# Kernel tuning notes

Measured on AMD Instinct MI355X. Metric: run time of the kernel, lower is better.

## Reference

```python
import jax, jax.numpy as jnp
import numpy as np

DIM = 256
HEADS = 8
WS = 7                      # window size
N = WS * WS                 # tokens per window = 49
SCALE = (DIM // HEADS) ** -0.5
B_ = 4096                   # total windows (64 images * 64 windows)
NW = 64                     # windows per image (mask.shape[0])


def _rel_index():
    # Swin relative position index, computed exactly as in the torch module.
    coords = np.stack(np.meshgrid(np.arange(WS), np.arange(WS), indexing='ij'))  # [2,WS,WS]
    cf = coords.reshape(2, -1)                          # [2, N]
    rel = cf[:, :, None] - cf[:, None, :]               # [2, N, N]
    rel = rel.transpose(1, 2, 0).copy()                 # [N, N, 2]
    rel[:, :, 0] += WS - 1
    rel[:, :, 1] += WS - 1
    rel[:, :, 0] *= 2 * WS - 1
    return rel.sum(-1)                                  # [N, N] in [0, (2WS-1)^2)


def setup_inputs() -> dict:
    key = jax.random.key(0)
    ks = jax.random.split(key, 7)
    x = jax.random.normal(ks[0], (B_, N, DIM), dtype=jnp.float32)
    mask = jax.random.normal(ks[1], (NW, N, N), dtype=jnp.float32)
    qkv_w = jax.random.normal(ks[2], (3 * DIM, DIM), dtype=jnp.float32) * 0.02
    qkv_b = jax.random.normal(ks[3], (3 * DIM,), dtype=jnp.float32) * 0.02
    proj_w = jax.random.normal(ks[4], (DIM, DIM), dtype=jnp.float32) * 0.02
    proj_b = jax.random.normal(ks[5], (DIM,), dtype=jnp.float32) * 0.02
    bias_table = jax.random.normal(ks[6], ((2 * WS - 1) ** 2, HEADS), dtype=jnp.float32) * 0.02
    rel_idx = jnp.asarray(_rel_index(), dtype=jnp.int32)
    return {"x": x, "mask": mask, "qkv_w": qkv_w, "qkv_b": qkv_b,
            "proj_w": proj_w, "proj_b": proj_b, "bias_table": bias_table,
            "rel_idx": rel_idx}


def reference(x, mask, qkv_w, qkv_b, proj_w, proj_b, bias_table, rel_idx):
    Bw, n, C = x.shape
    hd = C // HEADS
    # fused qkv projection: [Bw, n, 3C] -> [3, Bw, H, n, hd]
    qkv = (x @ qkv_w.T + qkv_b).reshape(Bw, n, 3, HEADS, hd).transpose(2, 0, 3, 1, 4)
    q, k, v = qkv[0] * SCALE, qkv[1], qkv[2]
    attn = jnp.einsum('bhnd,bhmd->bhnm', q, k)                     # [Bw,H,n,n]
    # relative position bias gather: [n*n, H] -> [H, n, n]
    bias = bias_table[rel_idx.reshape(-1)].reshape(n, n, HEADS).transpose(2, 0, 1)
    attn = attn + bias[None]
    nW = mask.shape[0]
    # shift mask add: group windows per image
    attn = attn.reshape(Bw // nW, nW, HEADS, n, n) + mask[None, :, None]
    attn = jax.nn.softmax(attn.reshape(Bw, HEADS, n, n), axis=-1)
    out = jnp.einsum('bhnm,bhmd->bhnd', attn, v)                   # [Bw,H,n,hd]
    out = out.transpose(0, 2, 1, 3).reshape(Bw, n, C)
    return out @ proj_w.T + proj_b
```

## Files before the change

kernel.cpp:

```cpp
#include <hip/hip_runtime.h>
#include <hip/hip_bf16.h>

#define NTOK 49
#define DIM 256
#define HEADS 8
#define HD 32
#define SCALE 0.17677669529663687f

typedef float f32x4 __attribute__((ext_vector_type(4)));
typedef short bf16x8 __attribute__((ext_vector_type(8)));

__device__ __forceinline__ unsigned short f2bf(float f) {
    union { __hip_bfloat16 h; unsigned short u; } c;
    c.h = __float2bfloat16(f);
    return c.u;
}
__device__ __forceinline__ float bf2f(unsigned short u) {
    return __builtin_bit_cast(float, (unsigned)u << 16);
}
__device__ __forceinline__ uint2 pack4(float a, float b, float c, float d) {
    uint2 r;
    r.x = (unsigned)f2bf(a) | ((unsigned)f2bf(b) << 16);
    r.y = (unsigned)f2bf(c) | ((unsigned)f2bf(d) << 16);
    return r;
}

__global__ void k0_prep(const float* __restrict__ qkv_w, const float* __restrict__ proj_w,
                        const float* __restrict__ mask, const float* __restrict__ bias_table,
                        const int* __restrict__ rel_idx,
                        unsigned short* __restrict__ wqf, unsigned short* __restrict__ wpf,
                        unsigned short* __restrict__ bmf, int total)
{
    int i = blockIdx.x * 256 + threadIdx.x;
    if (i >= total) return;
    if (i < 196608) {
        int j = i & 7, q = i >> 3;
        int lane = q & 63; q >>= 6;
        int ks2 = q & 7;  q >>= 3;
        int tt = q % 6;   q /= 6;
        int h  = q;
        int n96 = tt * 16 + (lane & 15);
        int seg = n96 >> 5, ch = n96 & 31;
        wqf[i] = f2bf(qkv_w[(seg * 256 + h * HD + ch) * 256 + ks2 * 32 + (lane >> 4) * 8 + j]);
    } else if (i < 262144) {
        int u = i - 196608;
        int j = u & 7, q = u >> 3;
        int lane = q & 63; q >>= 6;
        int ks2 = q & 7;  q >>= 3;
        int bt = q;
        int n = (bt >> 3) * 128 + (bt & 7) * 16 + (lane & 15);
        wpf[u] = f2bf(proj_w[n * 256 + ks2 * 32 + (lane >> 4) * 8 + j]);
    } else {
        int u = i - 262144;
        int j = u & 3;
        int lane = (u >> 2) & 63;
        int g = u >> 8;
        int mt = g & 3, ct = (g >> 2) & 3, h = (g >> 4) & 7, ws = g >> 7;
        int q = ct * 16 + (lane & 15);
        int key = mt * 16 + ((lane >> 4) & 3) * 4 + j;
        float v = 0.f;
        if (q < NTOK && key < NTOK)
            v = mask[ws * 2401 + q * NTOK + key] + bias_table[rel_idx[q * NTOK + key] * HEADS + h];
        bmf[u] = f2bf(v);
    }
}

__global__ __launch_bounds__(256, 2)
void k1_fused(
    const float* __restrict__ x,
    const float* __restrict__ qkv_b,
    const float* __restrict__ pb,
    const unsigned short* __restrict__ wqf,
    const unsigned short* __restrict__ wpf,
    const unsigned short* __restrict__ bmf,
    float* __restrict__ out)
{
    __shared__ unsigned short pool[37440];
    unsigned short* const xs = pool;

    const int t = threadIdx.x, bw = blockIdx.x;
    const int lane = t & 63, wv = t >> 6;
    const int l15 = lane & 15, l16 = lane >> 4;
    unsigned short* const qw  = pool + 12544 + wv * 6224;
    unsigned short* const kw  = qw + 1960;
    unsigned short* const vtw = qw + 3920;
    unsigned short* const pw2 = qw;

    const float* xw = x + (size_t)bw * NTOK * DIM;
    for (int cidx = t; cidx < NTOK * 32; cidx += 256) {
        int row = cidx >> 5, c8 = cidx & 31;
        float4 a = *(const float4*)(xw + row * DIM + c8 * 8);
        float4 b = *(const float4*)(xw + row * DIM + c8 * 8 + 4);
        bf16x8 v;
        v[0] = (short)f2bf(a.x); v[1] = (short)f2bf(a.y);
        v[2] = (short)f2bf(a.z); v[3] = (short)f2bf(a.w);
        v[4] = (short)f2bf(b.x); v[5] = (short)f2bf(b.y);
        v[6] = (short)f2bf(b.z); v[7] = (short)f2bf(b.w);
        *(bf16x8*)(xs + row * 256 + ((c8 * 8) ^ ((row & 7) << 3))) = v;
    }
    __syncthreads();

    int arow[4];
    #pragma unroll
    for (int i4 = 0; i4 < 4; ++i4) {
        int r = i4 * 16 + l15;
        arow[i4] = r > 48 ? 48 : r;
    }

    uint2 ob[2][2][4];

    #pragma unroll
    for (int hh = 0; hh < 2; ++hh) {
        const int h = wv + 4 * hh;
        const unsigned short* wb = wqf + (size_t)h * 24576;
        uint2 bmu[4][4];

        #pragma unroll
        for (int p = 0; p < 2; ++p) {
            f32x4 aq[4], ak[4], av[4];
            #pragma unroll
            for (int nt = 0; nt < 4; ++nt) {
                aq[nt] = (f32x4){0.f,0.f,0.f,0.f};
                ak[nt] = (f32x4){0.f,0.f,0.f,0.f};
                av[nt] = (f32x4){0.f,0.f,0.f,0.f};
            }
            __builtin_amdgcn_s_setprio(1);
            #pragma unroll
            for (int ks2 = 0; ks2 < 8; ++ks2) {
                bf16x8 xf[4];
                #pragma unroll
                for (int nt = 0; nt < 4; ++nt)
                    xf[nt] = *(const bf16x8*)(xs + arow[nt] * 256 +
                               ((ks2 * 32 + l16 * 8) ^ ((arow[nt] & 7) << 3)));
                bf16x8 wqf_ = *(const bf16x8*)(wb + ((p    ) * 8 + ks2) * 512 + lane * 8);
                bf16x8 wkf_ = *(const bf16x8*)(wb + ((2 + p) * 8 + ks2) * 512 + lane * 8);
                bf16x8 wvf_ = *(const bf16x8*)(wb + ((4 + p) * 8 + ks2) * 512 + lane * 8);
                #pragma unroll
                for (int nt = 0; nt < 4; ++nt) {
                    aq[nt] = __builtin_amdgcn_mfma_f32_16x16x32_bf16(wqf_, xf[nt], aq[nt], 0, 0, 0);
                    ak[nt] = __builtin_amdgcn_mfma_f32_16x16x32_bf16(wkf_, xf[nt], ak[nt], 0, 0, 0);
                    av[nt] = __builtin_amdgcn_mfma_f32_16x16x32_bf16(xf[nt], wvf_, av[nt], 0, 0, 0);
                }
            }
            __builtin_amdgcn_s_setprio(0);

            if (p == 0) {
                #pragma unroll
                for (int ct = 0; ct < 4; ++ct)
                    #pragma unroll
                    for (int mt = 0; mt < 4; ++mt)
                        bmu[ct][mt] = *(const uint2*)(bmf +
                            (((size_t)(((bw & 63) * 8 + h) * 16 + ct * 4 + mt)) << 8) + (lane << 2));
            }

            float4 bq4 = *(const float4*)(qkv_b + h * HD + p * 16 + l16 * 4);
            float4 bk4 = *(const float4*)(qkv_b + 256 + h * HD + p * 16 + l16 * 4);
            float  bvs = qkv_b[512 + h * HD + p * 16 + l15];
            #pragma unroll
            for (int nt = 0; nt < 4; ++nt) {
                int tok = nt * 16 + l15;
                if (tok < NTOK) {
                    *(uint2*)(qw + tok * 40 + p * 16 + l16 * 4) =
                        pack4((aq[nt][0] + bq4.x) * SCALE, (aq[nt][1] + bq4.y) * SCALE,
                              (aq[nt][2] + bq4.z) * SCALE, (aq[nt][3] + bq4.w) * SCALE);
                    *(uint2*)(kw + tok * 40 + p * 16 + l16 * 4) =
                        pack4(ak[nt][0] + bk4.x, ak[nt][1] + bk4.y,
                              ak[nt][2] + bk4.z, ak[nt][3] + bk4.w);
                }
                int ch = p * 16 + l15;
                int r0 = nt * 16 + l16 * 4;
                *(uint2*)(vtw + ch * 72 + r0) =
                    pack4(av[nt][0] + bvs, av[nt][1] + bvs, av[nt][2] + bvs, av[nt][3] + bvs);
            }
        }

        bf16x8 kf[4], qf[4];
        #pragma unroll
        for (int i4 = 0; i4 < 4; ++i4) {
            kf[i4] = *(const bf16x8*)(kw + arow[i4] * 40 + l16 * 8);
            qf[i4] = *(const bf16x8*)(qw + arow[i4] * 40 + l16 * 8);
        }

        #pragma unroll
        for (int ct = 0; ct < 4; ++ct) {
            f32x4 sT[4];
            __builtin_amdgcn_s_setprio(1);
            #pragma unroll
            for (int mt = 0; mt < 4; ++mt) {
                f32x4 z = (f32x4){0.f,0.f,0.f,0.f};
                sT[mt] = __builtin_amdgcn_mfma_f32_16x16x32_bf16(kf[mt], qf[ct], z, 0, 0, 0);
            }
            __builtin_amdgcn_s_setprio(0);

            float vv[4][4];
            float mx = -1e30f;
            #pragma unroll
            for (int mt = 0; mt < 4; ++mt) {
                float b0 = bf2f((unsigned short)(bmu[ct][mt].x & 0xffff));
                float b1 = bf2f((unsigned short)(bmu[ct][mt].x >> 16));
                float b2 = bf2f((unsigned short)(bmu[ct][mt].y & 0xffff));
                float b3 = bf2f((unsigned short)(bmu[ct][mt].y >> 16));
                float bj[4] = {b0, b1, b2, b3};
                #pragma unroll
                for (int j = 0; j < 4; ++j) {
                    float v = sT[mt][j] + bj[j];
                    if (mt * 16 + l16 * 4 + j >= NTOK) v = -1e30f;
                    vv[mt][j] = v;
                    mx = fmaxf(mx, v);
                }
            }
            mx = fmaxf(mx, __shfl_xor(mx, 16));
            mx = fmaxf(mx, __shfl_xor(mx, 32));
            float sum = 0.f;
            #pragma unroll
            for (int mt = 0; mt < 4; ++mt)
                #pragma unroll
                for (int j = 0; j < 4; ++j) {
                    float e = __expf(vv[mt][j] - mx);
                    vv[mt][j] = e;
                    sum += e;
                }
            sum += __shfl_xor(sum, 16);
            sum += __shfl_xor(sum, 32);
            float inv = 1.f / sum;
            int q = ct * 16 + l15;
            if (q < NTOK) {
                #pragma unroll
                for (int mt = 0; mt < 4; ++mt)
                    *(uint2*)(pw2 + q * 72 + mt * 16 + l16 * 4) =
                        pack4(vv[mt][0] * inv, vv[mt][1] * inv,
                              vv[mt][2] * inv, vv[mt][3] * inv);
            }
        }

        f32x4 o_[2][4];
        #pragma unroll
        for (int a = 0; a < 2; ++a)
            #pragma unroll
            for (int ct = 0; ct < 4; ++ct) o_[a][ct] = (f32x4){0.f,0.f,0.f,0.f};
        __builtin_amdgcn_s_setprio(1);
        #pragma unroll
        for (int kt = 0; kt < 2; ++kt) {
            bf16x8 pf[4];
            #pragma unroll
            for (int ct = 0; ct < 4; ++ct)
                pf[ct] = *(const bf16x8*)(pw2 + arow[ct] * 72 + kt * 32 + l16 * 8);
            #pragma unroll
            for (int a = 0; a < 2; ++a) {
                bf16x8 vf = *(const bf16x8*)(vtw + (a * 16 + l15) * 72 + kt * 32 + l16 * 8);
                #pragma unroll
                for (int ct = 0; ct < 4; ++ct)
                    o_[a][ct] = __builtin_amdgcn_mfma_f32_16x16x32_bf16(vf, pf[ct], o_[a][ct], 0, 0, 0);
            }
        }
        __builtin_amdgcn_s_setprio(0);

        #pragma unroll
        for (int a = 0; a < 2; ++a)
            #pragma unroll
            for (int ct = 0; ct < 4; ++ct)
                ob[hh][a][ct] = pack4(o_[a][ct][0], o_[a][ct][1], o_[a][ct][2], o_[a][ct][3]);
    }

    __syncthreads();

    #pragma unroll
    for (int hh = 0; hh < 2; ++hh) {
        #pragma unroll
        for (int a = 0; a < 2; ++a) {
            #pragma unroll
            for (int ct = 0; ct < 4; ++ct) {
                int tok = ct * 16 + l15;
                if (tok < NTOK) {
                    int ch0 = (wv + 4 * hh) * HD + a * 16 + l16 * 4;
                    int ad = tok * 256 + ((ch0 & ~7) ^ ((tok & 7) << 3)) + (ch0 & 7);
                    *(uint2*)(xs + ad) = ob[hh][a][ct];
                }
            }
        }
    }
    __syncthreads();

    f32x4 pacc[4][4];
    #pragma unroll
    for (int ct = 0; ct < 4; ++ct)
        #pragma unroll
        for (int u = 0; u < 4; ++u) pacc[ct][u] = (f32x4){0.f,0.f,0.f,0.f};

    __builtin_amdgcn_s_setprio(1);
    #pragma unroll
    for (int ks2 = 0; ks2 < 8; ++ks2) {
        bf16x8 xf[4];
        #pragma unroll
        for (int ct = 0; ct < 4; ++ct)
            xf[ct] = *(const bf16x8*)(xs + arow[ct] * 256 +
                       ((ks2 * 32 + l16 * 8) ^ ((arow[ct] & 7) << 3)));
        #pragma unroll
        for (int u = 0; u < 4; ++u) {
            bf16x8 wf = *(const bf16x8*)(wpf + (size_t)((wv * 4 + u) * 8 + ks2) * 512 + lane * 8);
            #pragma unroll
            for (int ct = 0; ct < 4; ++ct)
                pacc[ct][u] = __builtin_amdgcn_mfma_f32_16x16x32_bf16(wf, xf[ct], pacc[ct][u], 0, 0, 0);
        }
    }
    __builtin_amdgcn_s_setprio(0);

    #pragma unroll
    for (int u = 0; u < 4; ++u) {
        int bt = wv * 4 + u;
        int base = (bt >> 3) * 128 + (bt & 7) * 16;
        float4 pb4 = *(const float4*)(pb + base + l16 * 4);
        #pragma unroll
        for (int ct = 0; ct < 4; ++ct) {
            int tok = ct * 16 + l15;
            if (tok < NTOK) {
                float4 r;
                r.x = pacc[ct][u][0] + pb4.x;
                r.y = pacc[ct][u][1] + pb4.y;
                r.z = pacc[ct][u][2] + pb4.z;
                r.w = pacc[ct][u][3] + pb4.w;
                *(float4*)(out + ((size_t)bw * NTOK + tok) * DIM + base + l16 * 4) = r;
            }
        }
    }
}

extern "C" void kernel_launch(void* const* d_in, const int* in_sizes, int n_in,
                              void* d_out, int out_size, void* d_ws, size_t ws_size,
                              hipStream_t stream) {
    const float* x    = (const float*)d_in[0];
    const float* mask = (const float*)d_in[1];
    const float* qkvw = (const float*)d_in[2];
    const float* qkvb = (const float*)d_in[3];
    const float* pw   = (const float*)d_in[4];
    const float* pb   = (const float*)d_in[5];
    const float* bt   = (const float*)d_in[6];
    const int*   ri   = (const int*)d_in[7];
    float* out = (float*)d_out;

    unsigned short* wqf = (unsigned short*)d_ws;
    unsigned short* wpf = wqf + 196608;
    unsigned short* bmf = (unsigned short*)((char*)d_ws + 524288);

    const int nwin = in_sizes[0] / (NTOK * DIM);
    const int total = 262144 + 64 * HEADS * 16 * 256;

    k0_prep<<<(total + 255) / 256, 256, 0, stream>>>(qkvw, pw, mask, bt, ri,
                                                     wqf, wpf, bmf, total);
    k1_fused<<<nwin, 256, 0, stream>>>(x, qkvb, pb, wqf, wpf, bmf, out);
}
```

Measured before the change: 268.5 us.

## Keep Q/K/V/P in registers via 16x16x16 MFMA, drop LDS staging, raise occupancy

Instead of spilling Q, K, V^T and the softmax probabilities to per-wave LDS scratch and reloading them as 16x16x32 fragments, the kernel keeps the packed accumulator outputs in registers. It feeds them straight into 16x16x16 bf16 MFMAs, whose operand layout matches the accumulator layout. The PV product is now fused per query tile inside the softmax loop. LDS shrinks to only the x tile, so launch bounds go from 2 to 3 blocks per SIMD group, at the cost of more register pressure and twice as many smaller MFMA instructions.

```diff
diff --git a/kernel.cpp b/kernel.cpp
--- a/kernel.cpp
+++ b/kernel.cpp
@@ -9,6 +9,7 @@
 
 typedef float f32x4 __attribute__((ext_vector_type(4)));
 typedef short bf16x8 __attribute__((ext_vector_type(8)));
+typedef short bf16x4 __attribute__((ext_vector_type(4)));
 
 __device__ __forceinline__ unsigned short f2bf(float f) {
     union { __hip_bfloat16 h; unsigned short u; } c;
@@ -23,6 +24,21 @@
     r.x = (unsigned)f2bf(a) | ((unsigned)f2bf(b) << 16);
     r.y = (unsigned)f2bf(c) | ((unsigned)f2bf(d) << 16);
     return r;
+}
+
+__device__ __forceinline__ f32x4 mfma16(uint2 a, uint2 b, f32x4 c) {
+    bf16x4 av = __builtin_bit_cast(bf16x4, a);
+    bf16x4 bv = __builtin_bit_cast(bf16x4, b);
+#if __has_builtin(__builtin_amdgcn_mfma_f32_16x16x16bf16_1k)
+    return __builtin_amdgcn_mfma_f32_16x16x16bf16_1k(av, bv, c, 0, 0, 0);
+#elif __has_builtin(__builtin_amdgcn_mfma_f32_16x16x16_bf16)
+    return __builtin_amdgcn_mfma_f32_16x16x16_bf16(av, bv, c, 0, 0, 0);
+#else
+    f32x4 d;
+    asm volatile("v_mfma_f32_16x16x16_bf16 %0, %1, %2, %3"
+                 : "=v"(d) : "v"(av), "v"(bv), "v"(c));
+    return d;
+#endif
 }
 
 __global__ void k0_prep(const float* __restrict__ qkv_w, const float* __restrict__ proj_w,
@@ -65,7 +81,7 @@
     }
 }
 
-__global__ __launch_bounds__(256, 2)
+__global__ __launch_bounds__(256, 3)
 void k1_fused(
     const float* __restrict__ x,
     const float* __restrict__ qkv_b,
@@ -75,16 +91,11 @@
     const unsigned short* __restrict__ bmf,
     float* __restrict__ out)
 {
-    __shared__ unsigned short pool[37440];
-    unsigned short* const xs = pool;
+    __shared__ unsigned short xs[49 * 256];
 
     const int t = threadIdx.x, bw = blockIdx.x;
     const int lane = t & 63, wv = t >> 6;
     const int l15 = lane & 15, l16 = lane >> 4;
-    unsigned short* const qw  = pool + 12544 + wv * 6224;
-    unsigned short* const kw  = qw + 1960;
-    unsigned short* const vtw = qw + 3920;
-    unsigned short* const pw2 = qw;
 
     const float* xw = x + (size_t)bw * NTOK * DIM;
     for (int cidx = t; cidx < NTOK * 32; cidx += 256) {
@@ -113,6 +124,7 @@
     for (int hh = 0; hh < 2; ++hh) {
         const int h = wv + 4 * hh;
         const unsigned short* wb = wqf + (size_t)h * 24576;
+        uint2 qpk[4][2], kpk[4][2], vpk[4][2];
         uint2 bmu[4][4];
 
         #pragma unroll
@@ -144,7 +156,7 @@
             }
             __builtin_amdgcn_s_setprio(0);
 
-            if (p == 0) {
+            if (p == 1) {
                 #pragma unroll
                 for (int ct = 0; ct < 4; ++ct)
                     #pragma unroll
@@ -158,27 +170,13 @@
             float  bvs = qkv_b[512 + h * HD + p * 16 + l15];
             #pragma unroll
             for (int nt = 0; nt < 4; ++nt) {
-                int tok = nt * 16 + l15;
-                if (tok < NTOK) {
-                    *(uint2*)(qw + tok * 40 + p * 16 + l16 * 4) =
-                        pack4((aq[nt][0] + bq4.x) * SCALE, (aq[nt][1] + bq4.y) * SCALE,
-                              (aq[nt][2] + bq4.z) * SCALE, (aq[nt][3] + bq4.w) * SCALE);
-                    *(uint2*)(kw + tok * 40 + p * 16 + l16 * 4) =
-                        pack4(ak[nt][0] + bk4.x, ak[nt][1] + bk4.y,
-                              ak[nt][2] + bk4.z, ak[nt][3] + bk4.w);
-                }
-                int ch = p * 16 + l15;
-                int r0 = nt * 16 + l16 * 4;
-                *(uint2*)(vtw + ch * 72 + r0) =
-                    pack4(av[nt][0] + bvs, av[nt][1] + bvs, av[nt][2] + bvs, av[nt][3] + bvs);
-            }
-        }
-
-        bf16x8 kf[4], qf[4];
-        #pragma unroll
-        for (int i4 = 0; i4 < 4; ++i4) {
-            kf[i4] = *(const bf16x8*)(kw + arow[i4] * 40 + l16 * 8);
-            qf[i4] = *(const bf16x8*)(qw + arow[i4] * 40 + l16 * 8);
+                qpk[nt][p] = pack4((aq[nt][0] + bq4.x) * SCALE, (aq[nt][1] + bq4.y) * SCALE,
+                                   (aq[nt][2] + bq4.z) * SCALE, (aq[nt][3] + bq4.w) * SCALE);
+                kpk[nt][p] = pack4(ak[nt][0] + bk4.x, ak[nt][1] + bk4.y,
+                                   ak[nt][2] + bk4.z, ak[nt][3] + bk4.w);
+                vpk[nt][p] = pack4(av[nt][0] + bvs, av[nt][1] + bvs,
+                                   av[nt][2] + bvs, av[nt][3] + bvs);
+            }
         }
 
         #pragma unroll
@@ -188,7 +186,8 @@
             #pragma unroll
             for (int mt = 0; mt < 4; ++mt) {
                 f32x4 z = (f32x4){0.f,0.f,0.f,0.f};
-                sT[mt] = __builtin_amdgcn_mfma_f32_16x16x32_bf16(kf[mt], qf[ct], z, 0, 0, 0);
+                sT[mt] = mfma16(kpk[mt][1], qpk[ct][1],
+                                mfma16(kpk[mt][0], qpk[ct][0], z));
             }
             __builtin_amdgcn_s_setprio(0);
 
@@ -223,43 +222,25 @@
             sum += __shfl_xor(sum, 16);
             sum += __shfl_xor(sum, 32);
             float inv = 1.f / sum;
-            int q = ct * 16 + l15;
-            if (q < NTOK) {
-                #pragma unroll
-                for (int mt = 0; mt < 4; ++mt)
-                    *(uint2*)(pw2 + q * 72 + mt * 16 + l16 * 4) =
-                        pack4(vv[mt][0] * inv, vv[mt][1] * inv,
-                              vv[mt][2] * inv, vv[mt][3] * inv);
-            }
-        }
-
-        f32x4 o_[2][4];
-        #pragma unroll
-        for (int a = 0; a < 2; ++a)
-            #pragma unroll
-            for (int ct = 0; ct < 4; ++ct) o_[a][ct] = (f32x4){0.f,0.f,0.f,0.f};
-        __builtin_amdgcn_s_setprio(1);
-        #pragma unroll
-        for (int kt = 0; kt < 2; ++kt) {
-            bf16x8 pf[4];
-            #pragma unroll
-            for (int ct = 0; ct < 4; ++ct)
-                pf[ct] = *(const bf16x8*)(pw2 + arow[ct] * 72 + kt * 32 + l16 * 8);
-            #pragma unroll
-            for (int a = 0; a < 2; ++a) {
-                bf16x8 vf = *(const bf16x8*)(vtw + (a * 16 + l15) * 72 + kt * 32 + l16 * 8);
-                #pragma unroll
-                for (int ct = 0; ct < 4; ++ct)
-                    o_[a][ct] = __builtin_amdgcn_mfma_f32_16x16x32_bf16(vf, pf[ct], o_[a][ct], 0, 0, 0);
-            }
-        }
-        __builtin_amdgcn_s_setprio(0);
-
-        #pragma unroll
-        for (int a = 0; a < 2; ++a)
-            #pragma unroll
-            for (int ct = 0; ct < 4; ++ct)
-                ob[hh][a][ct] = pack4(o_[a][ct][0], o_[a][ct][1], o_[a][ct][2], o_[a][ct][3]);
+
+            uint2 ppk[4];
+            #pragma unroll
+            for (int mt = 0; mt < 4; ++mt)
+                ppk[mt] = pack4(vv[mt][0] * inv, vv[mt][1] * inv,
+                                vv[mt][2] * inv, vv[mt][3] * inv);
+
+            f32x4 o0 = (f32x4){0.f,0.f,0.f,0.f};
+            f32x4 o1 = (f32x4){0.f,0.f,0.f,0.f};
+            __builtin_amdgcn_s_setprio(1);
+            #pragma unroll
+            for (int mt = 0; mt < 4; ++mt) {
+                o0 = mfma16(vpk[mt][0], ppk[mt], o0);
+                o1 = mfma16(vpk[mt][1], ppk[mt], o1);
+            }
+            __builtin_amdgcn_s_setprio(0);
+            ob[hh][0][ct] = pack4(o0[0], o0[1], o0[2], o0[3]);
+            ob[hh][1][ct] = pack4(o1[0], o1[1], o1[2], o1[3]);
+        }
     }
 
     __syncthreads();
```

Result: no change. 265.7 us (-1.0%).
